# Kernel optimization log

Hardware: AMD Instinct MI355X
Metric: run time of the kernel (lower is better)

Reference implementation:

```python
import jax, jax.numpy as jnp
import numpy as np

# ---- static lookup-point config (matches cfg.radius/stride/level) ----
RADIUS = [4, 4, 4, 4]
STRIDE = [1, 1, 1, 1]
LEVEL = [0, 1, 2, 3]

def _build_pts():
    pts = {}
    for r, s, l in zip(RADIUS, STRIDE, LEVEL):
        pts.setdefault(l, set())
        for x in range(-r, r + 1):
            for y in range(-r, r + 1):
                pts[l].add((x * s, y * s))
    # sorted() reproduces torch's `v.sort()` on (x, y) tuples
    return {l: np.array(sorted(v), dtype=np.float32) for l, v in sorted(pts.items())}

PTS = _build_pts()                       # {lvl: (n_lvl, 2) offsets in level pixels}
N_LEVELS = max(LEVEL) + 1                # 4
CORR_DIM = 2 * sum(len(v) for v in PTS.values())   # 648
C_HALF = CORR_DIM // 2                   # 324 = per-direction channels
B, C, H, W = 1, 256, 80, 80


def _bilinear_sample(corr, x, y):
    """corr: (B, P, h, w); x, y: (P, n) pixel coords (align_corners=False convention,
    already converted to pixel space). Zero padding outside. Returns (B, P, n)."""
    Bn, P, h, w = corr.shape
    cf = corr.reshape(Bn, P, h * w)
    x0 = jnp.floor(x)
    y0 = jnp.floor(y)
    wx1 = x - x0
    wy1 = y - y0
    x0i = x0.astype(jnp.int32)
    y0i = y0.astype(jnp.int32)
    out = jnp.zeros((Bn, P, x.shape[-1]), corr.dtype)
    for dx, wxx in ((0, 1.0 - wx1), (1, wx1)):
        for dy, wyy in ((0, 1.0 - wy1), (1, wy1)):
            xi = x0i + dx
            yi = y0i + dy
            valid = (xi >= 0) & (xi < w) & (yi >= 0) & (yi < h)
            idx = jnp.clip(yi, 0, h - 1) * w + jnp.clip(xi, 0, w - 1)   # (P, n)
            v = jnp.take_along_axis(cf, jnp.broadcast_to(idx[None], (Bn,) + idx.shape), axis=2)
            out = out + v * (wxx * wyy * valid)[None]
    return out


def _lookup_pyramid(pyr):
    """pyr[lvl]: (B, P, H>>lvl, W>>lvl). Returns (B, P, C_HALF)."""
    outs = []
    for lvl, pts in PTS.items():
        s = 1 << lvl
        n = pts.shape[0]
        dxy = jnp.asarray(pts)
        # grid_sample align_corners=False: level-pixel coord of full-res pixel j is
        # (2j+1)/(2s) - 0.5; neighbor offsets are exactly `pts` in level pixels.
        bx = (2.0 * jnp.arange(W) + 1.0) / (2.0 * s) - 0.5   # (W,)
        by = (2.0 * jnp.arange(H) + 1.0) / (2.0 * s) - 0.5   # (H,)
        x = jnp.broadcast_to(bx[None, :, None] + dxy[None, None, :, 0], (H, W, n)).reshape(H * W, n)
        y = jnp.broadcast_to(by[:, None, None] + dxy[None, None, :, 1], (H, W, n)).reshape(H * W, n)
        outs.append(_bilinear_sample(pyr[lvl], x, y))
    return jnp.concatenate(outs, axis=-1)


def _pyramid(corr):
    """corr: (B, P, H, W) -> list of avg-pooled levels (2x2, stride 2)."""
    p = [corr]
    for _ in range(N_LEVELS - 1):
        b, pp, h, w = corr.shape
        corr = corr.reshape(b, pp, h // 2, 2, w // 2, 2).mean(axis=(3, 5))
        p.append(corr)
    return p


def _conv3x3_relu(x, w, b):
    y = jax.lax.conv_general_dilated(x, w, (1, 1), 'SAME',
                                     dimension_numbers=('NHWC', 'HWIO', 'NHWC'))
    return jax.nn.relu(y + b)


def _layer_norm(x, g, b, eps=1e-5):
    m = x.mean(-1, keepdims=True)
    v = ((x - m) ** 2).mean(-1, keepdims=True)
    return (x - m) * jax.lax.rsqrt(v + eps) * g + b


def setup_inputs() -> dict:
    key = jax.random.key(0)
    ks = jax.random.split(key, 4)
    return {
        'f0': jax.random.normal(ks[0], (B, C, H, W), jnp.float32),
        'f1': jax.random.normal(ks[1], (B, C, H, W), jnp.float32),
        'conv_w1': jax.random.normal(ks[2], (3, 3, C_HALF, C_HALF), jnp.float32) * 0.02,
        'conv_b1': jnp.zeros((C_HALF,), jnp.float32),
        'conv_w2': jax.random.normal(ks[3], (3, 3, C_HALF, C_HALF), jnp.float32) * 0.02,
        'conv_b2': jnp.zeros((C_HALF,), jnp.float32),
        'ln_g': jnp.ones((C_HALF,), jnp.float32),
        'ln_b': jnp.zeros((C_HALF,), jnp.float32),
    }


def reference(f0, f1, conv_w1, conv_b1, conv_w2, conv_b2, ln_g, ln_b):
    Bn, Cn, Hn, Wn = f0.shape
    P = Hn * Wn
    a = f0.reshape(Bn, Cn, P)
    bb = f1.reshape(Bn, Cn, P)
    corr01 = jnp.einsum('bcp,bcq->bpq', a, bb)          # (B, P, P)
    corr10 = jnp.swapaxes(corr01, 1, 2)
    feat01 = _lookup_pyramid(_pyramid(corr01.reshape(Bn, P, Hn, Wn)))   # (B, P, C_HALF)
    feat10 = _lookup_pyramid(_pyramid(corr10.reshape(Bn, P, Hn, Wn)))

    def branch(feat):
        x = feat.reshape(Bn, Hn, Wn, C_HALF)
        y = x + _conv3x3_relu(_conv3x3_relu(x, conv_w1, conv_b1), conv_w2, conv_b2)
        y = _layer_norm(y, ln_g, ln_b)
        return jnp.transpose(y, (0, 3, 1, 2))           # (B, C_HALF, H, W)

    return jnp.concatenate([branch(feat01), branch(feat10)], axis=1)    # (B, 2*C_HALF, H, W)
```

## Files before the change

### kernel.cpp

```cpp
#include <hip/hip_runtime.h>

typedef unsigned short u16;
typedef unsigned int   u32;
typedef float f32x4 __attribute__((ext_vector_type(4)));
typedef __bf16 bf16x8 __attribute__((ext_vector_type(8)));
typedef unsigned short u16x8 __attribute__((ext_vector_type(8)));

#define PP   6400
#define HH   80
#define WW   80
#define KC   256
#define CH   324
#define CPAD 384
#define PW   82
#define PPIX (PW*PW)
#define NP2  896

__device__ inline float b2f(u16 u) { union { u32 i; float f; } v; v.i = ((u32)u) << 16; return v.f; }
__device__ inline u16 f2b(float f) {
    union { u32 i; float f; } v; v.f = f;
    u32 r = v.i + 0x7fffu + ((v.i >> 16) & 1u);
    return (u16)(r >> 16);
}

__device__ __forceinline__ void gload16(const void* g, void* l) {
    __builtin_amdgcn_global_load_lds((const __attribute__((address_space(1))) void*)g,
                                     (__attribute__((address_space(3))) void*)l, 16, 0, 0);
}

__global__ __launch_bounds__(256) void prep_f(const float* __restrict__ f0,
                                              const float* __restrict__ f1,
                                              u16* __restrict__ fA, u16* __restrict__ fB) {
    __shared__ float tile[64][65];
    int p0 = blockIdx.x * 64, c0 = blockIdx.y * 64;
    const float* src = blockIdx.z ? f1 : f0;
    u16* dst = blockIdx.z ? fB : fA;
    int tid = threadIdx.x;
#pragma unroll
    for (int it = 0; it < 16; ++it) {
        int idx = tid + it * 256;
        int cc = idx >> 6, pp = idx & 63;
        tile[cc][pp] = src[(size_t)(c0 + cc) * PP + p0 + pp];
    }
    __syncthreads();
#pragma unroll
    for (int it = 0; it < 16; ++it) {
        int idx = tid + it * 256;
        int pp = idx >> 6, cc = idx & 63;
        dst[(size_t)(p0 + pp) * KC + c0 + cc] = f2b(tile[cc][pp]);
    }
}

__global__ __launch_bounds__(256) void prep_w(const float* __restrict__ w1,
                                              const float* __restrict__ w2,
                                              u16* __restrict__ wT1, u16* __restrict__ wT2) {
    __shared__ float tile[64][65];
    int tap = blockIdx.x;
    int t6 = blockIdx.y;
    int ci0 = (t6 / 6) * 64, co0 = (t6 % 6) * 64;
    const float* w = blockIdx.z ? w2 : w1;
    u16* wT = blockIdx.z ? wT2 : wT1;
    int tid = threadIdx.x;
#pragma unroll
    for (int it = 0; it < 16; ++it) {
        int idx = tid + it * 256;
        int ciL = idx >> 6, coL = idx & 63;
        int ci = ci0 + ciL, co = co0 + coL;
        tile[ciL][coL] = (ci < CH && co < CH) ? w[((size_t)tap * CH + ci) * CH + co] : 0.f;
    }
    __syncthreads();
#pragma unroll
    for (int it = 0; it < 16; ++it) {
        int idx = tid + it * 256;
        int coL = idx >> 6, ciL = idx & 63;
        wT[((size_t)tap * CPAD + co0 + coL) * CPAD + ci0 + ciL] = f2b(tile[ciL][coL]);
    }
}

__global__ __launch_bounds__(384) void zero_border(u16* __restrict__ feat, u16* __restrict__ t1,
                                                   const float* __restrict__ b1,
                                                   const float* __restrict__ b2,
                                                   float* __restrict__ b1p, float* __restrict__ b2p) {
    int bi = blockIdx.x, dir = blockIdx.y;
    int t = threadIdx.x;
    if (bi == 324) {
        if (dir == 0) b1p[t] = t < CH ? b1[t] : 0.f;
        else          b2p[t] = t < CH ? b2[t] : 0.f;
        return;
    }
    int pix;
    if (bi < 82) pix = bi;
    else if (bi < 164) pix = 81 * PW + (bi - 82);
    else if (bi < 244) pix = (bi - 164 + 1) * PW;
    else pix = (bi - 244 + 1) * PW + 81;
    size_t off = ((size_t)dir * PPIX + pix) * CPAD + t;
    feat[off] = 0;
    t1[off] = 0;
}

__global__ __launch_bounds__(256) void pool_feat(const u16* __restrict__ fA,
                                                 const u16* __restrict__ fB,
                                                 u16* __restrict__ pbarA,
                                                 u16* __restrict__ pbarB) {
    int j = blockIdx.x;
    const u16* src = blockIdx.y ? fA : fB;
    u16* dst = blockIdx.y ? pbarA : pbarB;
    int k = threadIdx.x;
    int cy3 = j / 10, cx3 = j % 10;
    float l1v[16], l2v[4];
#pragma unroll
    for (int a = 0; a < 4; ++a)
#pragma unroll
        for (int b = 0; b < 4; ++b) {
            int cy = cy3 * 4 + a, cx = cx3 * 4 + b;
            int p00 = (2 * cy) * 80 + 2 * cx;
            float v = 0.25f * (b2f(src[(size_t)p00 * KC + k]) + b2f(src[(size_t)(p00 + 1) * KC + k]) +
                               b2f(src[(size_t)(p00 + 80) * KC + k]) + b2f(src[(size_t)(p00 + 81) * KC + k]));
            l1v[a * 4 + b] = v;
            dst[(size_t)(cy * 40 + cx) * KC + k] = f2b(v);
        }
#pragma unroll
    for (int a = 0; a < 2; ++a)
#pragma unroll
        for (int b = 0; b < 2; ++b) {
            float v = 0.25f * (l1v[(2 * a) * 4 + 2 * b] + l1v[(2 * a) * 4 + 2 * b + 1] +
                               l1v[(2 * a + 1) * 4 + 2 * b] + l1v[(2 * a + 1) * 4 + 2 * b + 1]);
            l2v[a * 2 + b] = v;
            dst[(size_t)(1600 + (cy3 * 2 + a) * 20 + cx3 * 2 + b) * KC + k] = f2b(v);
        }
    float v3 = 0.25f * (l2v[0] + l2v[1] + l2v[2] + l2v[3]);
    dst[(size_t)(2000 + j) * KC + k] = f2b(v3);
}

__global__ __launch_bounds__(256) void gemm_cp(const u16* __restrict__ fA,
                                               const u16* __restrict__ fB,
                                               const u16* __restrict__ pbarA,
                                               const u16* __restrict__ pbarB,
                                               u16* __restrict__ pc,
                                               u16* __restrict__ feat) {
    int y = blockIdx.y, z = blockIdx.z;
    bool band = (y < 7);
    int m0 = blockIdx.x * 128, n0 = 0, jbase = 0;
    const u16 *Aptr, *Bptr;
    if (band) {
        if (z) return;
        int n0t = (int)blockIdx.x + y - 3;
        if (n0t < 0 || n0t >= 50) return;
        n0 = n0t * 128;
        Aptr = fA; Bptr = fB;
    } else {
        jbase = (y - 7) * 128;
        Aptr = z ? fB : fA;
        Bptr = z ? pbarA : pbarB;
    }
    int py0 = m0 / 80;
    int s1 = min(max(py0 / 2 - 5, 0), 28);
    int s2 = min(max(py0 / 4 - 5, 0), 8);

    __shared__ __align__(16) char smem[128 * 136 * 2];
    u16* As = (u16*)smem;
    u16* Bs = As + 128 * 64;
    u16* trans = (u16*)smem;
    const int TS = 136;
    int tid = threadIdx.x;
    int wave = tid >> 6, lane = tid & 63;
    int quad = lane >> 4, l16 = lane & 15;
    int lrow = lane >> 3, lchunk = lane & 7;
    int sc = lchunk ^ (lrow & 7);
    int sw = l16 & 7;
    int wr = (wave >> 1) * 64, wc = (wave & 1) * 64;
    f32x4 acc[4][4] = {};

    size_t gRow[4];
#pragma unroll
    for (int i = 0; i < 4; ++i) {
        int row = i * 32 + wave * 8 + lrow;
        if (band) gRow[i] = (size_t)(n0 + row);
        else {
            int j = jbase + row;
            int g = j < 480 ? s1 * 40 + j
                  : j < 720 ? 1120 + s2 * 20 + j
                  : j < 820 ? 1280 + j
                  : 2099;
            gRow[i] = (size_t)g;
        }
    }

    for (int k0 = 0; k0 < KC; k0 += 64) {
        __syncthreads();
#pragma unroll
        for (int i = 0; i < 4; ++i) {
            int row = i * 32 + wave * 8 + lrow;
            gload16(&Aptr[(size_t)(m0 + row) * KC + k0 + sc * 8], &As[(i * 32 + wave * 8) * 64]);
            gload16(&Bptr[gRow[i] * KC + k0 + sc * 8], &Bs[(i * 32 + wave * 8) * 64]);
        }
        __syncthreads();
#pragma unroll
        for (int ki = 0; ki < 2; ++ki) {
            bf16x8 af[4], bfr[4];
#pragma unroll
            for (int mi = 0; mi < 4; ++mi) {
                int r = wr + mi * 16 + l16;
                af[mi] = *(const bf16x8*)(&As[r * 64 + (((ki * 4 + quad) ^ sw) * 8)]);
            }
#pragma unroll
            for (int ni = 0; ni < 4; ++ni) {
                int r = wc + ni * 16 + l16;
                bfr[ni] = *(const bf16x8*)(&Bs[r * 64 + (((ki * 4 + quad) ^ sw) * 8)]);
            }
#pragma unroll
            for (int mi = 0; mi < 4; ++mi)
#pragma unroll
                for (int ni = 0; ni < 4; ++ni)
                    acc[mi][ni] = __builtin_amdgcn_mfma_f32_16x16x32_bf16(af[mi], bfr[ni], acc[mi][ni], 0, 0, 0);
        }
    }
    if (band) {
        u16* fd0 = feat;
        u16* fd1 = feat + (size_t)PPIX * CPAD;
#pragma unroll
        for (int ni = 0; ni < 4; ++ni) {
            int q = n0 + wc + ni * 16 + l16;
            int qy = q / 80, qx = q - qy * 80;
            size_t qpix = (size_t)((qy + 1) * PW + qx + 1) * CPAD;
#pragma unroll
            for (int mi = 0; mi < 4; ++mi)
#pragma unroll
                for (int rr = 0; rr < 4; ++rr) {
                    int p = m0 + wr + mi * 16 + quad * 4 + rr;
                    int py = p / 80, px = p - py * 80;
                    int dx = qx - px, dy = qy - py;
                    if ((unsigned)(dx + 4) < 9u && (unsigned)(dy + 4) < 9u) {
                        u16 v = f2b(acc[mi][ni][rr]);
                        size_t ppix = (size_t)((py + 1) * PW + px + 1) * CPAD;
                        fd0[ppix + (dx + 4) * 9 + (dy + 4)] = v;
                        fd1[qpix + (4 - dx) * 9 + (4 - dy)] = v;
                    }
                }
        }
        return;
    }
    __syncthreads();
#pragma unroll
    for (int mi = 0; mi < 4; ++mi)
#pragma unroll
        for (int ni = 0; ni < 4; ++ni) {
            int rbase = wr + mi * 16 + quad * 4;
            int c = wc + ni * 16 + l16;
#pragma unroll
            for (int rr = 0; rr < 4; ++rr)
                trans[(rbase + rr) * TS + c] = f2b(acc[mi][ni][rr]);
        }
    __syncthreads();
    {
        int dir = z;
#pragma unroll
        for (int it = 0; it < 8; ++it) {
            int r = it * 16 + (tid >> 4);
            int c8 = (tid & 15) * 8;
            u16x8 v = *(const u16x8*)(&trans[r * TS + c8]);
            *(u16x8*)(&pc[((size_t)dir * PP + m0 + r) * NP2 + jbase + c8]) = v;
        }
    }
}

__global__ __launch_bounds__(384) void lookup(const u16* __restrict__ pc,
                                              u16* __restrict__ feat) {
    __shared__ __align__(16) u16 pcrow[4][NP2];
    int p0 = blockIdx.x * 4, dir = blockIdx.y;
    int tid = threadIdx.x;
    int mt = p0 >> 7;
    int py0 = (mt * 128) / 80;
    int s1 = min(max(py0 / 2 - 5, 0), 28);
    int s2 = min(max(py0 / 4 - 5, 0), 8);
    for (int i = tid; i < 4 * (NP2 / 8); i += 384) {
        int j = i / (NP2 / 8), cc = i % (NP2 / 8);
        *(u16x8*)(&pcrow[j][cc * 8]) =
            *(const u16x8*)(&pc[((size_t)dir * PP + p0 + j) * NP2 + cc * 8]);
    }
    __syncthreads();
    int ch = tid;
#pragma unroll
    for (int j = 0; j < 4; ++j) {
        int p = p0 + j;
        int px = p % WW, py = p / WW;
        size_t pix = (size_t)(py + 1) * PW + px + 1;
        if (ch < 81) {
            int dx = ch / 9 - 4, dy = ch % 9 - 4;
            int x = px + dx, yy = py + dy;
            if ((unsigned)x >= (unsigned)WW || (unsigned)yy >= (unsigned)HH)
                feat[((size_t)dir * PPIX + pix) * CPAD + ch] = 0;
        } else if (ch < CH) {
            int lvl = ch / 81, i = ch % 81;
            int dx = i / 9 - 4, dy = i % 9 - 4;
            int wl = WW >> lvl;
            float inv = 1.0f / (float)(2 << lvl);
            float xc = (float)(2 * px + 1) * inv - 0.5f + (float)dx;
            float yc = (float)(2 * py + 1) * inv - 0.5f + (float)dy;
            float x0f = floorf(xc), y0f = floorf(yc);
            int x0 = (int)x0f, y0 = (int)y0f;
            float wx = xc - x0f, wy = yc - y0f;
            float val = 0.f;
#pragma unroll
            for (int cy = 0; cy < 2; ++cy)
#pragma unroll
                for (int cx = 0; cx < 2; ++cx) {
                    int xi = x0 + cx, yi = y0 + cy;
                    if ((unsigned)xi < (unsigned)wl && (unsigned)yi < (unsigned)wl) {
                        float wgt = (cx ? wx : 1.f - wx) * (cy ? wy : 1.f - wy);
                        int idx = (lvl == 1) ? (yi - s1) * 40 + xi
                                : (lvl == 2) ? 480 + (yi - s2) * 20 + xi
                                             : 720 + yi * 10 + xi;
                        val += b2f(pcrow[j][idx]) * wgt;
                    }
                }
            feat[((size_t)dir * PPIX + pix) * CPAD + ch] = f2b(val);
        } else {
            feat[((size_t)dir * PPIX + pix) * CPAD + ch] = 0;
        }
    }
}

__global__ __launch_bounds__(256) void conv_gemm(const u16* __restrict__ inFeat,
                                                 const u16* __restrict__ wTt,
                                                 const float* __restrict__ bias,
                                                 const u16* __restrict__ resid,
                                                 u16* __restrict__ outb) {
    int L = (int)blockIdx.x;
    int xcd = L & 7;
    int q = L >> 3;
    int n_t = q % 3; q /= 3;
    int mg = q % 13;
    int dir = q / 13;
    int m_t = mg * 8 + xcd;
    if (m_t >= 100) return;
    const u16* Ain = inFeat + (size_t)dir * PPIX * CPAD;
    const u16* Rin = resid ? resid + (size_t)dir * PPIX * CPAD : (const u16*)0;
    u16* Out = outb + (size_t)dir * PPIX * CPAD;
    __shared__ __align__(16) u16 As[64 * 128];
    __shared__ __align__(16) u16 Bs[128 * 128];
    int tid = threadIdx.x;
    int wave = tid >> 6, lane = tid & 63;
    int quad = lane >> 4, l16 = lane & 15;
    int wr = (wave >> 1) * 32, wc = (wave & 1) * 64;
    int m0 = m_t * 64, n0 = n_t * 128;
    f32x4 acc[2][4] = {};

    int pixA[4], scI[4];
#pragma unroll
    for (int i = 0; i < 4; ++i) {
        int r = wave * 16 + i * 4 + quad;
        int m = m0 + r;
        pixA[i] = (m / 80 + 1) * PW + (m % 80) + 1;
        scI[i] = l16 ^ ((i * 4 + quad) & 15);
    }

    for (int tap = 0; tap < 9; ++tap) {
        int dpix = (tap / 3 - 1) * PW + (tap % 3) - 1;
        const u16* Wt = wTt + ((size_t)tap * CPAD + n0) * CPAD;
#pragma unroll
        for (int kt = 0; kt < 3; ++kt) {
            int kc = kt * 128;
            __syncthreads();
#pragma unroll
            for (int i = 0; i < 4; ++i)
                gload16(&Ain[(size_t)(pixA[i] + dpix) * CPAD + kc + scI[i] * 8],
                        &As[(wave * 16 + i * 4) * 128]);
#pragma unroll
            for (int j = 0; j < 8; ++j) {
                int rb = wave * 32 + j * 4;
                gload16(&Wt[(size_t)(rb + quad) * CPAD + kc + scI[j & 3] * 8],
                        &Bs[rb * 128]);
            }
            __syncthreads();
#pragma unroll
            for (int ki = 0; ki < 4; ++ki) {
                int slot = (ki * 4 + quad) ^ l16;
                bf16x8 af[2], bfr[4];
#pragma unroll
                for (int mi = 0; mi < 2; ++mi)
                    af[mi] = *(const bf16x8*)(&As[(wr + mi * 16 + l16) * 128 + slot * 8]);
#pragma unroll
                for (int ni = 0; ni < 4; ++ni)
                    bfr[ni] = *(const bf16x8*)(&Bs[(wc + ni * 16 + l16) * 128 + slot * 8]);
#pragma unroll
                for (int mi = 0; mi < 2; ++mi)
#pragma unroll
                    for (int ni = 0; ni < 4; ++ni)
                        acc[mi][ni] = __builtin_amdgcn_mfma_f32_16x16x32_bf16(af[mi], bfr[ni], acc[mi][ni], 0, 0, 0);
            }
        }
    }
#pragma unroll
    for (int mi = 0; mi < 2; ++mi)
#pragma unroll
        for (int rr = 0; rr < 4; ++rr) {
            int p = m0 + wr + mi * 16 + quad * 4 + rr;
            size_t opix = (size_t)(p / 80 + 1) * PW + (p % 80) + 1;
#pragma unroll
            for (int ni = 0; ni < 4; ++ni) {
                int co = n0 + wc + ni * 16 + l16;
                float v = acc[mi][ni][rr] + bias[co];
                v = fmaxf(v, 0.f);
                if (Rin) v += b2f(Rin[opix * CPAD + co]);
                Out[opix * CPAD + co] = f2b(v);
            }
        }
}

__global__ __launch_bounds__(256) void ln_out(const u16* __restrict__ t2,
                                              const float* __restrict__ g,
                                              const float* __restrict__ b,
                                              float* __restrict__ out) {
    int dir = blockIdx.y;
    int p0 = blockIdx.x * 64;
    const u16* Y = t2 + (size_t)dir * PPIX * CPAD;
    __shared__ u16 buf[64 * 325];
    __shared__ float mean_s[64], inv_s[64];
    __shared__ float part[64][4][2];
    int tid = threadIdx.x;
    for (int idx = tid; idx < 64 * CH; idx += 256) {
        int pp = idx / CH, c = idx - pp * CH;
        int p = p0 + pp;
        size_t pix = (size_t)(p / 80 + 1) * PW + (p % 80) + 1;
        buf[pp * 325 + c] = Y[pix * CPAD + c];
    }
    __syncthreads();
    {
        int pp = tid >> 2, q = tid & 3;
        float s = 0.f, s2 = 0.f;
        for (int c = q; c < CH; c += 4) { float v = b2f(buf[pp * 325 + c]); s += v; s2 += v * v; }
        part[pp][q][0] = s; part[pp][q][1] = s2;
    }
    __syncthreads();
    if (tid < 64) {
        float s = 0.f, s2 = 0.f;
        for (int q = 0; q < 4; ++q) { s += part[tid][q][0]; s2 += part[tid][q][1]; }
        float m = s / (float)CH;
        float var = s2 / (float)CH - m * m;
        if (var < 0.f) var = 0.f;
        mean_s[tid] = m;
        inv_s[tid] = rsqrtf(var + 1e-5f);
    }
    __syncthreads();
    for (int idx = tid; idx < CH * 64; idx += 256) {
        int c = idx >> 6, pp = idx & 63;
        float v = (b2f(buf[pp * 325 + c]) - mean_s[pp]) * inv_s[pp] * g[c] + b[c];
        out[((size_t)(dir * CH + c)) * PP + p0 + pp] = v;
    }
}

extern "C" void kernel_launch(void* const* d_in, const int* in_sizes, int n_in,
                              void* d_out, int out_size, void* d_ws, size_t ws_size,
                              hipStream_t stream) {
    const float* f0  = (const float*)d_in[0];
    const float* f1  = (const float*)d_in[1];
    const float* w1  = (const float*)d_in[2];
    const float* b1  = (const float*)d_in[3];
    const float* w2  = (const float*)d_in[4];
    const float* b2  = (const float*)d_in[5];
    const float* lng = (const float*)d_in[6];
    const float* lnb = (const float*)d_in[7];
    float* out = (float*)d_out;

    char* ws = (char*)d_ws;
    size_t off = 0;
    auto alloc = [&](size_t bytes) -> char* {
        char* r = ws + off;
        off += (bytes + 511) & ~(size_t)511;
        return r;
    };
    u16* fA     = (u16*)alloc((size_t)PP * KC * 2);
    u16* fB     = (u16*)alloc((size_t)PP * KC * 2);
    u16* pc     = (u16*)alloc((size_t)2 * PP * NP2 * 2);
    u16* feat   = (u16*)alloc((size_t)2 * PPIX * CPAD * 2);
    u16* t1     = (u16*)alloc((size_t)2 * PPIX * CPAD * 2);
    u16* t2     = (u16*)alloc((size_t)2 * PPIX * CPAD * 2);
    u16* pbarA  = (u16*)alloc((size_t)2176 * KC * 2);
    u16* pbarB  = (u16*)alloc((size_t)2176 * KC * 2);
    u16* wT1    = (u16*)alloc((size_t)9 * CPAD * CPAD * 2);
    u16* wT2    = (u16*)alloc((size_t)9 * CPAD * CPAD * 2);
    float* b1p  = (float*)alloc(CPAD * 4);
    float* b2p  = (float*)alloc(CPAD * 4);

    prep_f<<<dim3(100, 4, 2), 256, 0, stream>>>(f0, f1, fA, fB);
    prep_w<<<dim3(9, 36, 2), 256, 0, stream>>>(w1, w2, wT1, wT2);
    zero_border<<<dim3(325, 2), 384, 0, stream>>>(feat, t1, b1, b2, b1p, b2p);
    pool_feat<<<dim3(100, 2), 256, 0, stream>>>(fA, fB, pbarA, pbarB);
    gemm_cp<<<dim3(50, 14, 2), 256, 0, stream>>>(fA, fB, pbarA, pbarB, pc, feat);
    lookup<<<dim3(1600, 2), 384, 0, stream>>>(pc, feat);
    conv_gemm<<<dim3(624), 256, 0, stream>>>(feat, wT1, b1p, (const u16*)0, t1);
    conv_gemm<<<dim3(624), 256, 0, stream>>>(t1, wT2, b2p, feat, t2);
    ln_out<<<dim3(100, 2), 256, 0, stream>>>(t2, lng, lnb, out);
}
```

Before: 246.0 us.

## Split conv GEMM K-reduction in two halves with separate combine kernel

```diff
diff --git a/kernel.cpp b/kernel.cpp
--- a/kernel.cpp
+++ b/kernel.cpp
@@ -321,74 +321,72 @@
     }
 }
 
-__global__ __launch_bounds__(256) void conv_gemm(const u16* __restrict__ inFeat,
-                                                 const u16* __restrict__ wTt,
-                                                 const float* __restrict__ bias,
-                                                 const u16* __restrict__ resid,
-                                                 u16* __restrict__ outb) {
+__global__ __launch_bounds__(256) void conv_ks(const u16* __restrict__ inFeat,
+                                               const u16* __restrict__ wTt,
+                                               float* __restrict__ part) {
     int L = (int)blockIdx.x;
     int xcd = L & 7;
     int q = L >> 3;
     int n_t = q % 3; q /= 3;
-    int mg = q % 13;
-    int dir = q / 13;
+    int mg = q % 13; q /= 13;
+    int dir = q & 1;
+    int kh = q >> 1;
     int m_t = mg * 8 + xcd;
     if (m_t >= 100) return;
     const u16* Ain = inFeat + (size_t)dir * PPIX * CPAD;
-    const u16* Rin = resid ? resid + (size_t)dir * PPIX * CPAD : (const u16*)0;
-    u16* Out = outb + (size_t)dir * PPIX * CPAD;
-    __shared__ __align__(16) u16 As[64 * 128];
-    __shared__ __align__(16) u16 Bs[128 * 128];
+    float* P = part + ((size_t)(kh * 2 + dir)) * PP * CPAD;
+    __shared__ __align__(16) u16 As[64 * 64];
+    __shared__ __align__(16) u16 Bs[128 * 64];
     int tid = threadIdx.x;
     int wave = tid >> 6, lane = tid & 63;
     int quad = lane >> 4, l16 = lane & 15;
+    int lrow = lane >> 3, lchunk = lane & 7;
+    int sc = lchunk ^ lrow;
+    int sw = l16 & 7;
     int wr = (wave >> 1) * 32, wc = (wave & 1) * 64;
     int m0 = m_t * 64, n0 = n_t * 128;
     f32x4 acc[2][4] = {};
 
-    int pixA[4], scI[4];
-#pragma unroll
-    for (int i = 0; i < 4; ++i) {
-        int r = wave * 16 + i * 4 + quad;
-        int m = m0 + r;
+    int pixA[2];
+#pragma unroll
+    for (int i = 0; i < 2; ++i) {
+        int m = m0 + i * 32 + wave * 8 + lrow;
         pixA[i] = (m / 80 + 1) * PW + (m % 80) + 1;
-        scI[i] = l16 ^ ((i * 4 + quad) & 15);
-    }
-
-    for (int tap = 0; tap < 9; ++tap) {
+    }
+    int bRow[4];
+#pragma unroll
+    for (int j = 0; j < 4; ++j) bRow[j] = n0 + j * 32 + wave * 8 + lrow;
+
+    int s0 = kh * 27, s1e = s0 + 27;
+    for (int s = s0; s < s1e; ++s) {
+        int tap = s / 6, kt = s - tap * 6;
         int dpix = (tap / 3 - 1) * PW + (tap % 3) - 1;
-        const u16* Wt = wTt + ((size_t)tap * CPAD + n0) * CPAD;
-#pragma unroll
-        for (int kt = 0; kt < 3; ++kt) {
-            int kc = kt * 128;
-            __syncthreads();
-#pragma unroll
-            for (int i = 0; i < 4; ++i)
-                gload16(&Ain[(size_t)(pixA[i] + dpix) * CPAD + kc + scI[i] * 8],
-                        &As[(wave * 16 + i * 4) * 128]);
-#pragma unroll
-            for (int j = 0; j < 8; ++j) {
-                int rb = wave * 32 + j * 4;
-                gload16(&Wt[(size_t)(rb + quad) * CPAD + kc + scI[j & 3] * 8],
-                        &Bs[rb * 128]);
-            }
-            __syncthreads();
-#pragma unroll
-            for (int ki = 0; ki < 4; ++ki) {
-                int slot = (ki * 4 + quad) ^ l16;
-                bf16x8 af[2], bfr[4];
-#pragma unroll
-                for (int mi = 0; mi < 2; ++mi)
-                    af[mi] = *(const bf16x8*)(&As[(wr + mi * 16 + l16) * 128 + slot * 8]);
+        const u16* Wt = wTt + (size_t)tap * CPAD * CPAD;
+        int kc = kt * 64;
+        __syncthreads();
+#pragma unroll
+        for (int i = 0; i < 2; ++i)
+            gload16(&Ain[(size_t)(pixA[i] + dpix) * CPAD + kc + sc * 8],
+                    &As[(i * 32 + wave * 8) * 64]);
+#pragma unroll
+        for (int j = 0; j < 4; ++j)
+            gload16(&Wt[(size_t)bRow[j] * CPAD + kc + sc * 8],
+                    &Bs[(j * 32 + wave * 8) * 64]);
+        __syncthreads();
+#pragma unroll
+        for (int ki = 0; ki < 2; ++ki) {
+            bf16x8 af[2], bfr[4];
+#pragma unroll
+            for (int mi = 0; mi < 2; ++mi)
+                af[mi] = *(const bf16x8*)(&As[(wr + mi * 16 + l16) * 64 + (((ki * 4 + quad) ^ sw) * 8)]);
+#pragma unroll
+            for (int ni = 0; ni < 4; ++ni)
+                bfr[ni] = *(const bf16x8*)(&Bs[(wc + ni * 16 + l16) * 64 + (((ki * 4 + quad) ^ sw) * 8)]);
+#pragma unroll
+            for (int mi = 0; mi < 2; ++mi)
 #pragma unroll
                 for (int ni = 0; ni < 4; ++ni)
-                    bfr[ni] = *(const bf16x8*)(&Bs[(wc + ni * 16 + l16) * 128 + slot * 8]);
-#pragma unroll
-                for (int mi = 0; mi < 2; ++mi)
-#pragma unroll
-                    for (int ni = 0; ni < 4; ++ni)
-                        acc[mi][ni] = __builtin_amdgcn_mfma_f32_16x16x32_bf16(af[mi], bfr[ni], acc[mi][ni], 0, 0, 0);
-            }
+                    acc[mi][ni] = __builtin_amdgcn_mfma_f32_16x16x32_bf16(af[mi], bfr[ni], acc[mi][ni], 0, 0, 0);
         }
     }
 #pragma unroll
@@ -396,16 +394,36 @@
 #pragma unroll
         for (int rr = 0; rr < 4; ++rr) {
             int p = m0 + wr + mi * 16 + quad * 4 + rr;
-            size_t opix = (size_t)(p / 80 + 1) * PW + (p % 80) + 1;
+            size_t base = (size_t)p * CPAD;
 #pragma unroll
             for (int ni = 0; ni < 4; ++ni) {
                 int co = n0 + wc + ni * 16 + l16;
-                float v = acc[mi][ni][rr] + bias[co];
-                v = fmaxf(v, 0.f);
-                if (Rin) v += b2f(Rin[opix * CPAD + co]);
-                Out[opix * CPAD + co] = f2b(v);
+                P[base + co] = acc[mi][ni][rr];
             }
         }
+}
+
+__global__ __launch_bounds__(256) void combine(const float* __restrict__ part,
+                                               const float* __restrict__ bias,
+                                               const u16* __restrict__ resid,
+                                               u16* __restrict__ outb) {
+    int idx = (int)blockIdx.x * 256 + threadIdx.x;
+    int pr = idx / 48, c8 = (idx - pr * 48) * 8;
+    int dir = pr >= PP;
+    int p = pr - dir * PP;
+    const float* P0 = part + (size_t)dir * PP * CPAD + (size_t)p * CPAD + c8;
+    const float* P1 = P0 + (size_t)2 * PP * CPAD;
+    size_t opix = ((size_t)(p / 80 + 1) * PW + (p % 80) + 1) * CPAD + c8;
+    const u16* R = resid ? resid + (size_t)dir * PPIX * CPAD + opix : (const u16*)0;
+    u16x8 ov;
+#pragma unroll
+    for (int k = 0; k < 8; ++k) {
+        float v = P0[k] + P1[k] + bias[c8 + k];
+        v = fmaxf(v, 0.f);
+        if (R) v += b2f(R[k]);
+        ov[k] = f2b(v);
+    }
+    *(u16x8*)(&outb[(size_t)dir * PPIX * CPAD + opix]) = ov;
 }
 
 __global__ __launch_bounds__(256) void ln_out(const u16* __restrict__ t2,
@@ -417,7 +435,7 @@
     const u16* Y = t2 + (size_t)dir * PPIX * CPAD;
     __shared__ u16 buf[64 * 325];
     __shared__ float mean_s[64], inv_s[64];
-    __shared__ float part[64][4][2];
+    __shared__ float part_s[64][4][2];
     int tid = threadIdx.x;
     for (int idx = tid; idx < 64 * CH; idx += 256) {
         int pp = idx / CH, c = idx - pp * CH;
@@ -430,12 +448,12 @@
         int pp = tid >> 2, q = tid & 3;
         float s = 0.f, s2 = 0.f;
         for (int c = q; c < CH; c += 4) { float v = b2f(buf[pp * 325 + c]); s += v; s2 += v * v; }
-        part[pp][q][0] = s; part[pp][q][1] = s2;
+        part_s[pp][q][0] = s; part_s[pp][q][1] = s2;
     }
     __syncthreads();
     if (tid < 64) {
         float s = 0.f, s2 = 0.f;
-        for (int q = 0; q < 4; ++q) { s += part[tid][q][0]; s2 += part[tid][q][1]; }
+        for (int q = 0; q < 4; ++q) { s += part_s[tid][q][0]; s2 += part_s[tid][q][1]; }
         float m = s / (float)CH;
         float var = s2 / (float)CH - m * m;
         if (var < 0.f) var = 0.f;
@@ -480,6 +498,7 @@
     u16* pbarB  = (u16*)alloc((size_t)2176 * KC * 2);
     u16* wT1    = (u16*)alloc((size_t)9 * CPAD * CPAD * 2);
     u16* wT2    = (u16*)alloc((size_t)9 * CPAD * CPAD * 2);
+    float* part = (float*)alloc((size_t)4 * PP * CPAD * 4);
     float* b1p  = (float*)alloc(CPAD * 4);
     float* b2p  = (float*)alloc(CPAD * 4);
 
@@ -489,7 +508,9 @@
     pool_feat<<<dim3(100, 2), 256, 0, stream>>>(fA, fB, pbarA, pbarB);
     gemm_cp<<<dim3(50, 14, 2), 256, 0, stream>>>(fA, fB, pbarA, pbarB, pc, feat);
     lookup<<<dim3(1600, 2), 384, 0, stream>>>(pc, feat);
-    conv_gemm<<<dim3(624), 256, 0, stream>>>(feat, wT1, b1p, (const u16*)0, t1);
-    conv_gemm<<<dim3(624), 256, 0, stream>>>(t1, wT2, b2p, feat, t2);
+    conv_ks<<<dim3(1248), 256, 0, stream>>>(feat, wT1, part);
+    combine<<<dim3(2400), 256, 0, stream>>>(part, b1p, (const u16*)0, t1);
+    conv_ks<<<dim3(1248), 256, 0, stream>>>(t1, wT2, part);
+    combine<<<dim3(2400), 256, 0, stream>>>(part, b2p, feat, t2);
     ln_out<<<dim3(100, 2), 256, 0, stream>>>(t2, lng, lnb, out);
 }
```

Result: slower. 322.9 us (+31.2%).
